# Kernel tuning notes

Hardware: AMD Instinct MI355X
Metric: run time of the kernel (lower is better)

## Reference

```python
import jax, jax.numpy as jnp
import numpy as np

# Graph sizes: each graph has exactly 32 nodes (forced by the rearrange + lin1 in_features)
BS = 4096
NODES = 32
N = BS * NODES          # 131072 total nodes
F_IN = 128
E_PER_G = 512
E = BS * E_PER_G        # 2097152 edges, all within-graph
HID = 1024
NCLS = 10


def setup_inputs() -> dict:
    key = jax.random.key(0)
    ks = jax.random.split(key, 9)
    x = jax.random.normal(ks[0], (N, F_IN), dtype=jnp.float32)
    # within-graph random edges: local node ids in [0,32) + per-graph offset
    graph_off = jnp.repeat(jnp.arange(BS, dtype=jnp.int64), E_PER_G) * NODES
    src = jax.random.randint(ks[1], (E,), 0, NODES, dtype=jnp.int64) + graph_off
    dst = jax.random.randint(ks[2], (E,), 0, NODES, dtype=jnp.int64) + graph_off
    edge_index = jnp.stack([src, dst], axis=0)
    s = 0.05
    gconv_w = jax.random.normal(ks[3], (F_IN, F_IN), dtype=jnp.float32) * s
    gconv_b = jax.random.normal(ks[4], (F_IN,), dtype=jnp.float32) * s
    lin1_w = jax.random.normal(ks[5], (HID, F_IN * NODES), dtype=jnp.float32) * s
    lin1_b = jax.random.normal(ks[6], (HID,), dtype=jnp.float32) * s
    lin2_w = jax.random.normal(ks[7], (NCLS, HID), dtype=jnp.float32) * s
    lin2_b = jax.random.normal(ks[8], (NCLS,), dtype=jnp.float32) * s
    return {"x": x, "edge_index": edge_index, "gconv_w": gconv_w,
            "gconv_b": gconv_b, "lin1_w": lin1_w, "lin1_b": lin1_b,
            "lin2_w": lin2_w, "lin2_b": lin2_b, "bs": BS}


def reference(x, edge_index, gconv_w, gconv_b, lin1_w, lin1_b, lin2_w, lin2_b, bs):
    # GINConv (eps=0): h_i = Linear( x_i + sum_{j->i} x_j )
    src, dst = edge_index[0], edge_index[1]
    agg = jax.ops.segment_sum(x[src], dst, num_segments=x.shape[0])  # [N, F]
    h = (x + agg) @ gconv_w.T + gconv_b                               # [N, F]
    h = jax.nn.relu(h)
    # rearrange '(bs e) f -> bs (f e)' with e=32 nodes per graph
    f = h.shape[-1]
    h = h.reshape(bs, NODES, f).transpose(0, 2, 1).reshape(bs, f * NODES)
    h = h @ lin1_w.T + lin1_b
    # dropout is identity in eval mode
    h = jax.nn.relu(h)
    h = h @ lin2_w.T + lin2_b
    return jax.nn.softmax(h, axis=-1)
```

## Files before the change

kernel.cpp:

```cpp
#include <hip/hip_runtime.h>

typedef _Float16 half_t;
typedef _Float16 halfv8 __attribute__((ext_vector_type(8)));
typedef _Float16 halfv4 __attribute__((ext_vector_type(4)));
typedef float    floatv4 __attribute__((ext_vector_type(4)));
typedef unsigned int uint;
typedef uint uintv4 __attribute__((ext_vector_type(4)));

#define NODES 32
#define FIN   128
#define EPG   512
#define NBS   4096
#define ETOT  (NBS*EPG)
#define HID   1024
#define KDIM  4096
#define NCLS  10
#define YP    36
#define WP    140

#define BM 256
#define BN 256
#define BK 64
#define KS 4
#define KSLEN (KDIM/KS)
#define NT (KSLEN/BK)

#define GLDS16(g, l)                                                        \
  __builtin_amdgcn_global_load_lds(                                         \
      (const __attribute__((address_space(1))) unsigned int*)(g),           \
      (__attribute__((address_space(3))) unsigned int*)(l), 16, 0, 0)

__global__ __launch_bounds__(256) void prep_cvt(const float* __restrict__ w1,
                                                half_t* __restrict__ w1p,
                                                const float* __restrict__ gw,
                                                half_t* __restrict__ gw16) {
  const size_t q = (size_t)blockIdx.x * 256 + threadIdx.x;
  const float* s;
  half_t* d;
  size_t off;
  if (q < 1048576) { s = w1; d = w1p; off = q; }
  else             { s = gw; d = gw16; off = q - 1048576; }
  floatv4 v = *(const floatv4*)(s + off * 4);
  halfv4 h = {(half_t)v[0], (half_t)v[1], (half_t)v[2], (half_t)v[3]};
  *(halfv4*)(d + off * 4) = h;
}

__global__ __launch_bounds__(256, 2) void gin_fused(
    const float* __restrict__ x, const int* __restrict__ ei,
    const half_t* __restrict__ gw16, const float* __restrict__ gb,
    half_t* __restrict__ H) {
  __shared__ __attribute__((aligned(16))) half_t Ws[FIN * WP];
  __shared__ __attribute__((aligned(16))) half_t Yt[4][FIN * YP];
  __shared__ uint cnt[4][512];

  const int t = threadIdx.x, w = t >> 6, l = t & 63;
  const int lr = l & 15, lk = l >> 4;
  const int g = blockIdx.x * 4 + w;

  const float* xg = x + (size_t)g * (NODES * FIN);
  floatv4 xr[2][4][2];
#pragma unroll
  for (int mt = 0; mt < 2; ++mt)
#pragma unroll
    for (int kk = 0; kk < 4; ++kk) {
      const float* p = xg + (mt * 16 + lr) * FIN + kk * 32 + lk * 8;
      xr[mt][kk][0] = *(const floatv4*)p;
      xr[mt][kk][1] = *(const floatv4*)(p + 4);
    }

  {
    const halfv8* gsrc = (const halfv8*)gw16;
#pragma unroll
    for (int i = 0; i < 8; ++i) {
      const int c = i * 256 + t;
      const int o = c >> 4, f8 = c & 15;
      *(halfv8*)&Ws[o * WP + f8 * 8] = gsrc[c];
    }
  }

  const int* sp = ei + (size_t)g * EPG;
  const int* dp = ei + (size_t)ETOT + (size_t)g * EPG;
  uintv4 s0 = *(const uintv4*)(sp + l * 8);
  uintv4 s1 = *(const uintv4*)(sp + l * 8 + 4);
  uintv4 d0 = *(const uintv4*)(dp + l * 8);
  uintv4 d1 = *(const uintv4*)(dp + l * 8 + 4);

  {
    uintv4* c4 = (uintv4*)cnt[w];
    uintv4 z = {0, 0, 0, 0};
    c4[l] = z;
    c4[l + 64] = z;
  }
#pragma unroll
  for (int q = 0; q < 4; ++q) {
    uint p0 = (d0[q] & 31) * 32 + (s0[q] & 31);
    atomicAdd(&cnt[w][p0 >> 1], 1u << ((p0 & 1) * 16));
    uint p1 = (d1[q] & 31) * 32 + (s1[q] & 31);
    atomicAdd(&cnt[w][p1 >> 1], 1u << ((p1 & 1) * 16));
  }

  halfv8 af[2][4];
#pragma unroll
  for (int mt = 0; mt < 2; ++mt)
#pragma unroll
    for (int kk = 0; kk < 4; ++kk) {
      halfv8 h;
#pragma unroll
      for (int q = 0; q < 4; ++q) {
        h[q]     = (half_t)xr[mt][kk][0][q];
        h[q + 4] = (half_t)xr[mt][kk][1][q];
      }
      af[mt][kk] = h;
    }

  __syncthreads();

  floatv4 acc[2][8] = {};
#pragma unroll
  for (int kk = 0; kk < 4; ++kk) {
    halfv8 bfk[8];
#pragma unroll
    for (int nt = 0; nt < 8; ++nt)
      bfk[nt] = *(const halfv8*)&Ws[(nt * 16 + lr) * WP + kk * 32 + lk * 8];
#pragma unroll
    for (int nt = 0; nt < 8; ++nt)
#pragma unroll
      for (int mt = 0; mt < 2; ++mt)
        acc[mt][nt] = __builtin_amdgcn_mfma_f32_16x16x32_f16(af[mt][kk], bfk[nt],
                                                             acc[mt][nt], 0, 0, 0);
  }
  __builtin_amdgcn_sched_barrier(0);

  half_t* yw = Yt[w];
#pragma unroll
  for (int mt = 0; mt < 2; ++mt)
#pragma unroll
    for (int nt = 0; nt < 8; ++nt) {
      halfv4 h = {(half_t)acc[mt][nt][0], (half_t)acc[mt][nt][1],
                  (half_t)acc[mt][nt][2], (half_t)acc[mt][nt][3]};
      *(halfv4*)&yw[(nt * 16 + lr) * YP + mt * 16 + lk * 4] = h;
    }

  const unsigned short* c16 = (const unsigned short*)cnt[w];
  halfv8 am[2];
#pragma unroll
  for (int mt = 0; mt < 2; ++mt) {
    const int i = mt * 16 + lr;
#pragma unroll
    for (int q = 0; q < 8; ++q) {
      const int j = lk * 8 + q;
      float c = (float)c16[i * 32 + j] + ((j == i) ? 1.f : 0.f);
      am[mt][q] = (half_t)c;
    }
  }

  floatv4 acc2[2][8] = {};
#pragma unroll
  for (int nt = 0; nt < 8; ++nt) {
    halfv8 bf = *(const halfv8*)&yw[(nt * 16 + lr) * YP + lk * 8];
#pragma unroll
    for (int mt = 0; mt < 2; ++mt)
      acc2[mt][nt] = __builtin_amdgcn_mfma_f32_16x16x32_f16(am[mt], bf,
                                                            acc2[mt][nt], 0, 0, 0);
  }
  __builtin_amdgcn_sched_barrier(0);

#pragma unroll
  for (int nt = 0; nt < 8; ++nt) {
    const float bias = gb[nt * 16 + lr];
#pragma unroll
    for (int mt = 0; mt < 2; ++mt) {
      halfv4 h;
#pragma unroll
      for (int q = 0; q < 4; ++q) {
        const float v = acc2[mt][nt][q] + bias;
        h[q] = (half_t)(v > 0.f ? v : 0.f);
      }
      *(halfv4*)&yw[(nt * 16 + lr) * YP + mt * 16 + lk * 4] = h;
    }
  }
  __builtin_amdgcn_sched_barrier(0);

  half_t* Hg = H + (size_t)g * KDIM;
#pragma unroll
  for (int c = 0; c < 8; ++c) {
    const int ch = c * 64 + l;
    const int o = ch >> 2, m0 = (ch & 3) * 8;
    halfv8 v = *(const halfv8*)&yw[o * YP + m0];
    *(halfv8*)(Hg + ch * 8) = v;
  }
}

__global__ __launch_bounds__(512, 2) void lin1_gemm(
    const half_t* __restrict__ A, const half_t* __restrict__ B,
    half_t* __restrict__ Cbase) {
  __shared__ __attribute__((aligned(16))) half_t As[2][BM * BK];
  __shared__ __attribute__((aligned(16))) half_t Bs[2][BN * BK];

  const int t = threadIdx.x;
  const int orig = blockIdx.x;
  const int wg = (orig & 7) * 32 + (orig >> 3);
  const int mt = wg & 15, rest = wg >> 4;
  const int nt_ = rest & 3, ks = rest >> 2;
  const int m0 = mt * BM, n0 = nt_ * BN, k0 = ks * KSLEN;

  const half_t* gA[4];
  const half_t* gB[4];
#pragma unroll
  for (int j = 0; j < 4; ++j) {
    const int L = t + j * 512;
    const int r = L >> 3;
    const int c = (L & 7) ^ (r & 7);
    gA[j] = A + (size_t)(m0 + r) * KDIM + k0 + c * 8;
    gB[j] = B + (size_t)(n0 + r) * KDIM + k0 + c * 8;
  }

#define STAGE(buf, koff)                                                    \
  {                                                                         \
    _Pragma("unroll")                                                       \
    for (int j = 0; j < 4; ++j)                                             \
      GLDS16(gA[j] + (koff), &As[buf][(t + j * 512) * 8]);                  \
    _Pragma("unroll")                                                       \
    for (int j = 0; j < 4; ++j)                                             \
      GLDS16(gB[j] + (koff), &Bs[buf][(t + j * 512) * 8]);                  \
  }

  const int w = t >> 6, l = t & 63, lr = l & 15, lk = l >> 4;
  const int wm = (w >> 2) * 128, wn = (w & 3) * 64;

  floatv4 acc[8][4] = {};

  STAGE(0, 0)
  STAGE(1, BK)
  asm volatile("s_waitcnt vmcnt(8)" ::: "memory");
  __builtin_amdgcn_s_barrier();

  for (int kt = 0; kt < NT; ++kt) {
    const int cur = kt & 1;
    const half_t* as = As[cur];
    const half_t* bs = Bs[cur];
#pragma unroll
    for (int ksb = 0; ksb < 2; ++ksb) {
      halfv8 bf[4], af[8];
#pragma unroll
      for (int nf = 0; nf < 4; ++nf) {
        const int row = wn + nf * 16 + lr;
        const int ch = (ksb * 4 + lk) ^ (row & 7);
        bf[nf] = *(const halfv8*)&bs[row * BK + ch * 8];
      }
#pragma unroll
      for (int mf = 0; mf < 8; ++mf) {
        const int row = wm + mf * 16 + lr;
        const int ch = (ksb * 4 + lk) ^ (row & 7);
        af[mf] = *(const halfv8*)&as[row * BK + ch * 8];
      }
      __builtin_amdgcn_s_setprio(1);
#pragma unroll
      for (int mf = 0; mf < 8; ++mf)
#pragma unroll
        for (int nf = 0; nf < 4; ++nf)
          acc[mf][nf] = __builtin_amdgcn_mfma_f32_16x16x32_f16(
              af[mf], bf[nf], acc[mf][nf], 0, 0, 0);
      __builtin_amdgcn_s_setprio(0);
    }
    __builtin_amdgcn_s_barrier();
    const int src = (kt + 2 < NT) ? (kt + 2) : 0;
    STAGE(cur, src * BK)
    asm volatile("s_waitcnt vmcnt(8)" ::: "memory");
    __builtin_amdgcn_s_barrier();
  }

  half_t* C = Cbase + (size_t)ks * ((size_t)NBS * HID);
#pragma unroll
  for (int mf = 0; mf < 8; ++mf)
#pragma unroll
    for (int nf = 0; nf < 4; ++nf) {
      const int n = n0 + wn + nf * 16 + lr;
#pragma unroll
      for (int q = 0; q < 4; ++q) {
        const int m = m0 + wm + mf * 16 + lk * 4 + q;
        C[(size_t)m * HID + n] = (half_t)acc[mf][nf][q];
      }
    }
#undef STAGE
}

__global__ __launch_bounds__(256) void head(
    const half_t* __restrict__ Cb, const float* __restrict__ b1,
    const float* __restrict__ w2, const float* __restrict__ b2,
    float* __restrict__ out) {
  __shared__ __attribute__((aligned(16))) float w2s[NCLS * HID];
  const int t = threadIdx.x;
  {
    const floatv4* s4 = (const floatv4*)w2;
    floatv4* d4 = (floatv4*)w2s;
    for (int i = t; i < (NCLS * HID) / 4; i += 256) d4[i] = s4[i];
  }
  __syncthreads();
  const int w = t >> 6, l = t & 63;
  const int row = blockIdx.x * 4 + w;

  float r[16];
#pragma unroll
  for (int jj = 0; jj < 4; ++jj) {
    floatv4 bb = *(const floatv4*)&b1[jj * 256 + l * 4];
    float s[4] = {bb[0], bb[1], bb[2], bb[3]};
#pragma unroll
    for (int p = 0; p < KS; ++p) {
      const half_t* cp = Cb + (size_t)p * ((size_t)NBS * HID) + (size_t)row * HID;
      halfv4 u = *(const halfv4*)&cp[jj * 256 + l * 4];
#pragma unroll
      for (int q = 0; q < 4; ++q) s[q] += (float)u[q];
    }
#pragma unroll
    for (int q = 0; q < 4; ++q) r[jj * 4 + q] = s[q] > 0.f ? s[q] : 0.f;
  }
  float lg[10];
#pragma unroll
  for (int c = 0; c < NCLS; ++c) {
    float p = 0.f;
#pragma unroll
    for (int jj = 0; jj < 4; ++jj) {
      floatv4 wv = *(const floatv4*)&w2s[c * HID + jj * 256 + l * 4];
      p += r[jj * 4 + 0] * wv[0] + r[jj * 4 + 1] * wv[1] +
           r[jj * 4 + 2] * wv[2] + r[jj * 4 + 3] * wv[3];
    }
#pragma unroll
    for (int off = 32; off >= 1; off >>= 1) p += __shfl_xor(p, off);
    lg[c] = p + b2[c];
  }
  float mx = lg[0];
#pragma unroll
  for (int c = 1; c < NCLS; ++c) mx = fmaxf(mx, lg[c]);
  float sum = 0.f;
#pragma unroll
  for (int c = 0; c < NCLS; ++c) { lg[c] = __expf(lg[c] - mx); sum += lg[c]; }
  const float inv = 1.f / sum;
  float myv = 0.f;
#pragma unroll
  for (int c = 0; c < NCLS; ++c) myv = (l == c) ? lg[c] * inv : myv;
  if (l < NCLS) out[(size_t)row * NCLS + l] = myv;
}

extern "C" void kernel_launch(void* const* d_in, const int* in_sizes, int n_in,
                              void* d_out, int out_size, void* d_ws, size_t ws_size,
                              hipStream_t stream) {
  (void)in_sizes; (void)n_in; (void)out_size; (void)ws_size;
  const float* x  = (const float*)d_in[0];
  const int*   ei = (const int*)d_in[1];
  const float* gw = (const float*)d_in[2];
  const float* gb = (const float*)d_in[3];
  const float* w1 = (const float*)d_in[4];
  const float* b1 = (const float*)d_in[5];
  const float* w2 = (const float*)d_in[6];
  const float* b2 = (const float*)d_in[7];
  float* out = (float*)d_out;

  char* ws = (char*)d_ws;
  half_t* H    = (half_t*)(ws);
  half_t* C    = (half_t*)(ws + 33554432);
  half_t* w1p  = (half_t*)(ws + 67108864);
  half_t* gw16 = (half_t*)(ws + 75497472);

  prep_cvt <<<dim3(4112),    dim3(256), 0, stream>>>(w1, w1p, gw, gw16);
  gin_fused<<<dim3(NBS / 4), dim3(256), 0, stream>>>(x, ei, gw16, gb, H);
  lin1_gemm<<<dim3(16 * 4 * KS), dim3(512), 0, stream>>>(H, w1p, C);
  head     <<<dim3(NBS / 4), dim3(256), 0, stream>>>(C, b1, w2, b2, out);
}
```

Before: 86.72 us.

## Split lin1 GEMM tiles into halves and interleave staging with quadrant MFMAs

Restructures the lin1 GEMM main loop so the A and B shared tiles are split into 128-row halves. Each half is loaded separately and interleaved with four quadrant MFMA phases, each behind its own barrier, instead of staging a whole buffer after all compute. The aim is finer-grained overlap of global-to-LDS loads with matrix-core work and less stall at the single per-iteration barrier. It adds more barriers and relies on tight vmcnt and lgkmcnt accounting, which risks hazards if the counts are wrong.

```diff
diff --git a/kernel.cpp b/kernel.cpp
--- a/kernel.cpp
+++ b/kernel.cpp
@@ -194,83 +194,144 @@
 __global__ __launch_bounds__(512, 2) void lin1_gemm(
     const half_t* __restrict__ A, const half_t* __restrict__ B,
     half_t* __restrict__ Cbase) {
-  __shared__ __attribute__((aligned(16))) half_t As[2][BM * BK];
-  __shared__ __attribute__((aligned(16))) half_t Bs[2][BN * BK];
+  __shared__ __attribute__((aligned(16))) half_t As[2 * 2 * 8192];
+  __shared__ __attribute__((aligned(16))) half_t Bs[2 * 2 * 8192];
 
   const int t = threadIdx.x;
   const int orig = blockIdx.x;
   const int wg = (orig & 7) * 32 + (orig >> 3);
   const int mt = wg & 15, rest = wg >> 4;
-  const int nt_ = rest & 3, ks = rest >> 2;
-  const int m0 = mt * BM, n0 = nt_ * BN, k0 = ks * KSLEN;
-
-  const half_t* gA[4];
-  const half_t* gB[4];
-#pragma unroll
-  for (int j = 0; j < 4; ++j) {
-    const int L = t + j * 512;
-    const int r = L >> 3;
-    const int c = (L & 7) ^ (r & 7);
-    gA[j] = A + (size_t)(m0 + r) * KDIM + k0 + c * 8;
-    gB[j] = B + (size_t)(n0 + r) * KDIM + k0 + c * 8;
-  }
-
-#define STAGE(buf, koff)                                                    \
-  {                                                                         \
-    _Pragma("unroll")                                                       \
-    for (int j = 0; j < 4; ++j)                                             \
-      GLDS16(gA[j] + (koff), &As[buf][(t + j * 512) * 8]);                  \
-    _Pragma("unroll")                                                       \
-    for (int j = 0; j < 4; ++j)                                             \
-      GLDS16(gB[j] + (koff), &Bs[buf][(t + j * 512) * 8]);                  \
-  }
+  const int nt_ = rest & 3, ksz = rest >> 2;
+  const int m0 = mt * BM, n0 = nt_ * BN, k0 = ksz * KSLEN;
+
+  const int srow0 = t >> 3, c_ = t & 7;
+  const int cs0 = (c_ ^ (srow0 & 7)) * 8;
+  const int srow1 = srow0 + 64;
+  const int cs1 = (c_ ^ (srow1 & 7)) * 8;
+  const half_t* gA[2][2] = {
+      {A + (size_t)(m0 + srow0) * KDIM + k0 + cs0,
+       A + (size_t)(m0 + srow1) * KDIM + k0 + cs1},
+      {A + (size_t)(m0 + 128 + srow0) * KDIM + k0 + cs0,
+       A + (size_t)(m0 + 128 + srow1) * KDIM + k0 + cs1}};
+  const half_t* gB[2][2] = {
+      {B + (size_t)(n0 + srow0) * KDIM + k0 + cs0,
+       B + (size_t)(n0 + srow1) * KDIM + k0 + cs1},
+      {B + (size_t)(n0 + 128 + srow0) * KDIM + k0 + cs0,
+       B + (size_t)(n0 + 128 + srow1) * KDIM + k0 + cs1}};
+
+#define STG_A(buf, hf, kk)                                                   \
+  { GLDS16(gA[hf][0] + (kk) * BK, &As[(buf) * 16384 + (hf) * 8192 + t * 8]); \
+    GLDS16(gA[hf][1] + (kk) * BK,                                            \
+           &As[(buf) * 16384 + (hf) * 8192 + (t + 512) * 8]); }
+#define STG_B(buf, hf, kk)                                                   \
+  { GLDS16(gB[hf][0] + (kk) * BK, &Bs[(buf) * 16384 + (hf) * 8192 + t * 8]); \
+    GLDS16(gB[hf][1] + (kk) * BK,                                            \
+           &Bs[(buf) * 16384 + (hf) * 8192 + (t + 512) * 8]); }
 
   const int w = t >> 6, l = t & 63, lr = l & 15, lk = l >> 4;
   const int wm = (w >> 2) * 128, wn = (w & 3) * 64;
+  const int ah = wm >> 7;
+  const int bh = wn >> 7;
+  const int bro = (wn & 64) + lr;
+  const int rsw = lr & 7;
 
   floatv4 acc[8][4] = {};
 
-  STAGE(0, 0)
-  STAGE(1, BK)
-  asm volatile("s_waitcnt vmcnt(8)" ::: "memory");
-  __builtin_amdgcn_s_barrier();
+  STG_B(0, 0, 0) STG_A(0, 0, 0) STG_A(0, 1, 0) STG_B(0, 1, 0)
+  STG_B(1, 0, 1) STG_A(1, 0, 1)
 
   for (int kt = 0; kt < NT; ++kt) {
-    const int cur = kt & 1;
-    const half_t* as = As[cur];
-    const half_t* bs = Bs[cur];
-#pragma unroll
-    for (int ksb = 0; ksb < 2; ++ksb) {
-      halfv8 bf[4], af[8];
-#pragma unroll
-      for (int nf = 0; nf < 4; ++nf) {
-        const int row = wn + nf * 16 + lr;
-        const int ch = (ksb * 4 + lk) ^ (row & 7);
-        bf[nf] = *(const halfv8*)&bs[row * BK + ch * 8];
-      }
-#pragma unroll
-      for (int mf = 0; mf < 8; ++mf) {
-        const int row = wm + mf * 16 + lr;
-        const int ch = (ksb * 4 + lk) ^ (row & 7);
-        af[mf] = *(const halfv8*)&as[row * BK + ch * 8];
-      }
-      __builtin_amdgcn_s_setprio(1);
-#pragma unroll
-      for (int mf = 0; mf < 8; ++mf)
-#pragma unroll
-        for (int nf = 0; nf < 4; ++nf)
+    const int cur = kt & 1, nxt = cur ^ 1;
+    const int kA = (kt + 1) & 15, kB = (kt + 2) & 15;
+    halfv8 af[4][2], bfA[2][2], bfB[2][2];
+
+    asm volatile("s_waitcnt vmcnt(4)" ::: "memory");
+    __builtin_amdgcn_s_barrier();
+    __builtin_amdgcn_sched_barrier(0);
+    STG_A(nxt, 1, kA)
+#pragma unroll
+    for (int mf = 0; mf < 4; ++mf)
+#pragma unroll
+      for (int ks = 0; ks < 2; ++ks)
+        af[mf][ks] = *(const halfv8*)&As[cur * 16384 + ah * 8192 +
+                                         (mf * 16 + lr) * 64 +
+                                         (((ks * 4 + lk) ^ rsw) * 8)];
+#pragma unroll
+    for (int nf = 0; nf < 2; ++nf)
+#pragma unroll
+      for (int ks = 0; ks < 2; ++ks)
+        bfA[nf][ks] = *(const halfv8*)&Bs[cur * 16384 + bh * 8192 +
+                                          (bro + nf * 16) * 64 +
+                                          (((ks * 4 + lk) ^ rsw) * 8)];
+    __builtin_amdgcn_s_setprio(1);
+#pragma unroll
+    for (int mf = 0; mf < 4; ++mf)
+#pragma unroll
+      for (int nf = 0; nf < 2; ++nf)
+#pragma unroll
+        for (int ks = 0; ks < 2; ++ks)
           acc[mf][nf] = __builtin_amdgcn_mfma_f32_16x16x32_f16(
-              af[mf], bf[nf], acc[mf][nf], 0, 0, 0);
-      __builtin_amdgcn_s_setprio(0);
-    }
+              af[mf][ks], bfA[nf][ks], acc[mf][nf], 0, 0, 0);
+    __builtin_amdgcn_s_setprio(0);
+
+    STG_B(nxt, 1, kA)
+#pragma unroll
+    for (int nf = 0; nf < 2; ++nf)
+#pragma unroll
+      for (int ks = 0; ks < 2; ++ks)
+        bfB[nf][ks] = *(const halfv8*)&Bs[cur * 16384 + bh * 8192 +
+                                          (bro + 32 + nf * 16) * 64 +
+                                          (((ks * 4 + lk) ^ rsw) * 8)];
+    __builtin_amdgcn_s_setprio(1);
+#pragma unroll
+    for (int mf = 0; mf < 4; ++mf)
+#pragma unroll
+      for (int nf = 0; nf < 2; ++nf)
+#pragma unroll
+        for (int ks = 0; ks < 2; ++ks)
+          acc[mf][nf + 2] = __builtin_amdgcn_mfma_f32_16x16x32_f16(
+              af[mf][ks], bfB[nf][ks], acc[mf][nf + 2], 0, 0, 0);
+    __builtin_amdgcn_s_setprio(0);
+
+    asm volatile("s_waitcnt lgkmcnt(0)" ::: "memory");
     __builtin_amdgcn_s_barrier();
-    const int src = (kt + 2 < NT) ? (kt + 2) : 0;
-    STAGE(cur, src * BK)
-    asm volatile("s_waitcnt vmcnt(8)" ::: "memory");
+    __builtin_amdgcn_sched_barrier(0);
+    STG_B(cur, 0, kB)
+#pragma unroll
+    for (int mf = 0; mf < 4; ++mf)
+#pragma unroll
+      for (int ks = 0; ks < 2; ++ks)
+        af[mf][ks] = *(const halfv8*)&As[cur * 16384 + ah * 8192 +
+                                         (64 + mf * 16 + lr) * 64 +
+                                         (((ks * 4 + lk) ^ rsw) * 8)];
+    __builtin_amdgcn_s_setprio(1);
+#pragma unroll
+    for (int mf = 0; mf < 4; ++mf)
+#pragma unroll
+      for (int nf = 0; nf < 2; ++nf)
+#pragma unroll
+        for (int ks = 0; ks < 2; ++ks)
+          acc[mf + 4][nf] = __builtin_amdgcn_mfma_f32_16x16x32_f16(
+              af[mf][ks], bfA[nf][ks], acc[mf + 4][nf], 0, 0, 0);
+    __builtin_amdgcn_s_setprio(0);
+
+    asm volatile("s_waitcnt lgkmcnt(0)" ::: "memory");
     __builtin_amdgcn_s_barrier();
-  }
-
-  half_t* C = Cbase + (size_t)ks * ((size_t)NBS * HID);
+    __builtin_amdgcn_sched_barrier(0);
+    STG_A(cur, 0, kB)
+    __builtin_amdgcn_s_setprio(1);
+#pragma unroll
+    for (int mf = 0; mf < 4; ++mf)
+#pragma unroll
+      for (int nf = 0; nf < 2; ++nf)
+#pragma unroll
+        for (int ks = 0; ks < 2; ++ks)
+          acc[mf + 4][nf + 2] = __builtin_amdgcn_mfma_f32_16x16x32_f16(
+              af[mf][ks], bfB[nf][ks], acc[mf + 4][nf + 2], 0, 0, 0);
+    __builtin_amdgcn_s_setprio(0);
+  }
+
+  half_t* C = Cbase + (size_t)ksz * ((size_t)NBS * HID);
 #pragma unroll
   for (int mf = 0; mf < 8; ++mf)
 #pragma unroll
@@ -282,7 +343,8 @@
         C[(size_t)m * HID + n] = (half_t)acc[mf][nf][q];
       }
     }
-#undef STAGE
+#undef STG_A
+#undef STG_B
 }
 
 __global__ __launch_bounds__(256) void head(
```

Result: slower. 90.93 us (+4.9%).

## Restructure lin1 GEMM into 4-buffer BK=32 pipeline with interleaved loads

Applied to the files above, without the earlier changes.

Halves the K tile to 32, uses four LDS buffers with a prefetch distance of two, and issues the next tile's global-to-LDS loads in the middle of the MFMA sequence. This removes one of the two barriers per iteration. It also switches to a new XOR swizzle suited to 32-element rows. The intent is to overlap memory traffic with matrix math and cut the barrier stall. The cost is twice as many loop iterations and barriers overall, and more reliance on the vmcnt accounting being correct.

```diff
diff --git a/kernel.cpp b/kernel.cpp
--- a/kernel.cpp
+++ b/kernel.cpp
@@ -20,7 +20,7 @@
 
 #define BM 256
 #define BN 256
-#define BK 64
+#define BK 32
 #define KS 4
 #define KSLEN (KDIM/KS)
 #define NT (KSLEN/BK)
@@ -29,6 +29,10 @@
   __builtin_amdgcn_global_load_lds(                                         \
       (const __attribute__((address_space(1))) unsigned int*)(g),           \
       (__attribute__((address_space(3))) unsigned int*)(l), 16, 0, 0)
+
+__device__ __forceinline__ int qidx(int row, int c) {
+  return row * 32 + ((c ^ ((row >> 1) & 3)) * 8);
+}
 
 __global__ __launch_bounds__(256) void prep_cvt(const float* __restrict__ w1,
                                                 half_t* __restrict__ w1p,
@@ -194,83 +198,87 @@
 __global__ __launch_bounds__(512, 2) void lin1_gemm(
     const half_t* __restrict__ A, const half_t* __restrict__ B,
     half_t* __restrict__ Cbase) {
-  __shared__ __attribute__((aligned(16))) half_t As[2][BM * BK];
-  __shared__ __attribute__((aligned(16))) half_t Bs[2][BN * BK];
+  __shared__ __attribute__((aligned(16))) half_t As[4][8192];
+  __shared__ __attribute__((aligned(16))) half_t Bs[4][8192];
 
   const int t = threadIdx.x;
   const int orig = blockIdx.x;
   const int wg = (orig & 7) * 32 + (orig >> 3);
   const int mt = wg & 15, rest = wg >> 4;
-  const int nt_ = rest & 3, ks = rest >> 2;
-  const int m0 = mt * BM, n0 = nt_ * BN, k0 = ks * KSLEN;
-
-  const half_t* gA[4];
-  const half_t* gB[4];
-#pragma unroll
-  for (int j = 0; j < 4; ++j) {
-    const int L = t + j * 512;
-    const int r = L >> 3;
-    const int c = (L & 7) ^ (r & 7);
-    gA[j] = A + (size_t)(m0 + r) * KDIM + k0 + c * 8;
-    gB[j] = B + (size_t)(n0 + r) * KDIM + k0 + c * 8;
-  }
-
-#define STAGE(buf, koff)                                                    \
-  {                                                                         \
-    _Pragma("unroll")                                                       \
-    for (int j = 0; j < 4; ++j)                                             \
-      GLDS16(gA[j] + (koff), &As[buf][(t + j * 512) * 8]);                  \
-    _Pragma("unroll")                                                       \
-    for (int j = 0; j < 4; ++j)                                             \
-      GLDS16(gB[j] + (koff), &Bs[buf][(t + j * 512) * 8]);                  \
-  }
+  const int nt_ = rest & 3, ksz = rest >> 2;
+  const int m0 = mt * BM, n0 = nt_ * BN, k0 = ksz * KSLEN;
+
+  const half_t* gA[2];
+  const half_t* gB[2];
+#pragma unroll
+  for (int j = 0; j < 2; ++j) {
+    const int p = t + j * 512;
+    const int r = p >> 2, c = p & 3;
+    const int cs = (c ^ ((r >> 1) & 3)) * 8;
+    gA[j] = A + (size_t)(m0 + r) * KDIM + k0 + cs;
+    gB[j] = B + (size_t)(n0 + r) * KDIM + k0 + cs;
+  }
+
+#define STG_A(buf, kt_)                                                      \
+  { GLDS16(gA[0] + (kt_) * BK, &As[buf][t * 8]);                             \
+    GLDS16(gA[1] + (kt_) * BK, &As[buf][(t + 512) * 8]); }
+#define STG_B(buf, kt_)                                                      \
+  { GLDS16(gB[0] + (kt_) * BK, &Bs[buf][t * 8]);                             \
+    GLDS16(gB[1] + (kt_) * BK, &Bs[buf][(t + 512) * 8]); }
 
   const int w = t >> 6, l = t & 63, lr = l & 15, lk = l >> 4;
   const int wm = (w >> 2) * 128, wn = (w & 3) * 64;
 
   floatv4 acc[8][4] = {};
 
-  STAGE(0, 0)
-  STAGE(1, BK)
-  asm volatile("s_waitcnt vmcnt(8)" ::: "memory");
+  STG_A(0, 0) STG_B(0, 0) STG_A(1, 1) STG_B(1, 1)
+  asm volatile("s_waitcnt vmcnt(4)" ::: "memory");
   __builtin_amdgcn_s_barrier();
+  __builtin_amdgcn_sched_barrier(0);
 
   for (int kt = 0; kt < NT; ++kt) {
-    const int cur = kt & 1;
+    const int cur = kt & 3;
+    const int nb = (kt + 2) & 3;
+    const int ktn = (kt + 2) & (NT - 1);
     const half_t* as = As[cur];
     const half_t* bs = Bs[cur];
-#pragma unroll
-    for (int ksb = 0; ksb < 2; ++ksb) {
-      halfv8 bf[4], af[8];
-#pragma unroll
-      for (int nf = 0; nf < 4; ++nf) {
-        const int row = wn + nf * 16 + lr;
-        const int ch = (ksb * 4 + lk) ^ (row & 7);
-        bf[nf] = *(const halfv8*)&bs[row * BK + ch * 8];
-      }
-#pragma unroll
-      for (int mf = 0; mf < 8; ++mf) {
-        const int row = wm + mf * 16 + lr;
-        const int ch = (ksb * 4 + lk) ^ (row & 7);
-        af[mf] = *(const halfv8*)&as[row * BK + ch * 8];
-      }
-      __builtin_amdgcn_s_setprio(1);
-#pragma unroll
-      for (int mf = 0; mf < 8; ++mf)
-#pragma unroll
-        for (int nf = 0; nf < 4; ++nf)
-          acc[mf][nf] = __builtin_amdgcn_mfma_f32_16x16x32_f16(
-              af[mf], bf[nf], acc[mf][nf], 0, 0, 0);
-      __builtin_amdgcn_s_setprio(0);
-    }
+    halfv8 af[8], bfL[2], bfH[2];
+
+#pragma unroll
+    for (int mf = 0; mf < 8; ++mf)
+      af[mf] = *(const halfv8*)&as[qidx(wm + mf * 16 + lr, lk)];
+#pragma unroll
+    for (int nf = 0; nf < 2; ++nf)
+      bfL[nf] = *(const halfv8*)&bs[qidx(wn + nf * 16 + lr, lk)];
+    STG_A(nb, ktn)
+    __builtin_amdgcn_s_setprio(1);
+#pragma unroll
+    for (int mf = 0; mf < 8; ++mf)
+#pragma unroll
+      for (int nf = 0; nf < 2; ++nf)
+        acc[mf][nf] = __builtin_amdgcn_mfma_f32_16x16x32_f16(
+            af[mf], bfL[nf], acc[mf][nf], 0, 0, 0);
+    __builtin_amdgcn_s_setprio(0);
+
+#pragma unroll
+    for (int nf = 0; nf < 2; ++nf)
+      bfH[nf] = *(const halfv8*)&bs[qidx(wn + 32 + nf * 16 + lr, lk)];
+    STG_B(nb, ktn)
+    __builtin_amdgcn_s_setprio(1);
+#pragma unroll
+    for (int mf = 0; mf < 8; ++mf)
+#pragma unroll
+      for (int nf = 0; nf < 2; ++nf)
+        acc[mf][nf + 2] = __builtin_amdgcn_mfma_f32_16x16x32_f16(
+            af[mf], bfH[nf], acc[mf][nf + 2], 0, 0, 0);
+    __builtin_amdgcn_s_setprio(0);
+
+    asm volatile("s_waitcnt vmcnt(4)" ::: "memory");
     __builtin_amdgcn_s_barrier();
-    const int src = (kt + 2 < NT) ? (kt + 2) : 0;
-    STAGE(cur, src * BK)
-    asm volatile("s_waitcnt vmcnt(8)" ::: "memory");
-    __builtin_amdgcn_s_barrier();
-  }
-
-  half_t* C = Cbase + (size_t)ks * ((size_t)NBS * HID);
+    __builtin_amdgcn_sched_barrier(0);
+  }
+
+  half_t* C = Cbase + (size_t)ksz * ((size_t)NBS * HID);
 #pragma unroll
   for (int mf = 0; mf < 8; ++mf)
 #pragma unroll
@@ -282,7 +290,8 @@
         C[(size_t)m * HID + n] = (half_t)acc[mf][nf][q];
       }
     }
-#undef STAGE
+#undef STG_A
+#undef STG_B
 }
 
 __global__ __launch_bounds__(256) void head(
```

Measured after the change: 82.31 us. -5.1%, faster.
